# Performance work log

Measured on AMD Instinct MI355X. Metric: run time of the kernel, lower is better.

## Reference

```python
import jax, jax.numpy as jnp
import numpy as np

B, S, D, E, K = 4, 2048, 1024, 8, 2
H = 4 * D  # FFN hidden per expert


def setup_inputs() -> dict:
    key = jax.random.key(0)
    ks = jax.random.split(key, 5)
    s = 0.02  # init scale
    return {
        "x": jax.random.normal(ks[0], (B, S, D), dtype=jnp.float32),
        "Wg": jax.random.normal(ks[1], (D, E), dtype=jnp.float32) * s,
        "bg": jnp.zeros((E,), dtype=jnp.float32),
        "W1": jax.random.normal(ks[2], (E, D, H), dtype=jnp.float32) * s,
        "b1": jnp.zeros((E, H), dtype=jnp.float32),
        "W2": jax.random.normal(ks[3], (E, H, D), dtype=jnp.float32) * s,
        "b2": jnp.zeros((E, D), dtype=jnp.float32),
    }


def reference(x, Wg, bg, W1, b1, W2, b2):
    # Router: softmax over expert logits, then top-k (torch.topk semantics)
    probs = jax.nn.softmax(x @ Wg + bg, axis=-1)      # [B,S,E]
    w, idx = jax.lax.top_k(probs, K)                   # [B,S,K] each
    # Dense all-experts MLP (matches original: every expert runs on every token)
    h = jax.nn.gelu(jnp.einsum('bsd,edh->bseh', x, W1) + b1, approximate=False)  # [B,S,E,H]
    y = jnp.einsum('bseh,ehd->bsed', h, W2) + b2       # [B,S,E,D]
    # One-hot mask + weighted sum == gather selected experts, scale by w, sum over k
    yk = jnp.take_along_axis(y, idx[..., None], axis=2)  # [B,S,K,D]
    return jnp.sum(yk * w[..., None], axis=2)            # [B,S,D]
```

## Files before the change

### kernel.cpp

```cpp
#include <hip/hip_runtime.h>
#include <hip/hip_bf16.h>
#include <math.h>


#define TOK     8192
#define DMODEL  1024
#define NEXP    8
#define HFF     4096
#define NASSIGN 16384
#define SLOTPAD 16512
#define BM      128
#define BN      128
#define BK      32
#define MAXRT   135

typedef __attribute__((ext_vector_type(8))) short s16x8;
typedef __attribute__((ext_vector_type(4))) float f32x4;

__device__ __forceinline__ void gll16(const void* g, void* l) {
  __builtin_amdgcn_global_load_lds((const __attribute__((address_space(1))) void*)g,
                                   (__attribute__((address_space(3))) void*)l, 16, 0, 0);
}

__global__ void transpose_cvt(const float* __restrict__ in, __hip_bfloat16* __restrict__ out,
                              int R, int C) {
  __shared__ float t[64][65];
  const float* src = in + (size_t)blockIdx.z * R * C;
  __hip_bfloat16* dst = out + (size_t)blockIdx.z * R * C;
  const int r0 = blockIdx.y * 64, c0 = blockIdx.x * 64;
  const int tc = threadIdx.x & 63, tr = threadIdx.x >> 6;
#pragma unroll
  for (int i = 0; i < 16; ++i) {
    int r = i * 4 + tr;
    t[r][tc] = src[(size_t)(r0 + r) * C + c0 + tc];
  }
  __syncthreads();
#pragma unroll
  for (int i = 0; i < 16; ++i) {
    int rr = i * 4 + tr;
    dst[(size_t)(c0 + rr) * R + r0 + tc] = __float2bfloat16(t[tc][rr]);
  }
}

__global__ void router_kernel(const float* __restrict__ x, const float* __restrict__ Wg,
                              const float* __restrict__ bg, int* __restrict__ idx,
                              float* __restrict__ wtok, int* __restrict__ counts) {
  __shared__ int scnt[NEXP];
  if (threadIdx.x < NEXP) scnt[threadIdx.x] = 0;
  __syncthreads();
  const int wave = threadIdx.x >> 6, lane = threadIdx.x & 63;
  const int t = blockIdx.x * 4 + wave;
  float acc[NEXP];
#pragma unroll
  for (int e = 0; e < NEXP; ++e) acc[e] = 0.f;
  const float* xr = x + (size_t)t * DMODEL + lane * 16;
#pragma unroll
  for (int j = 0; j < 4; ++j) {
    float4 xv = *(const float4*)(xr + j * 4);
    const float* wr = Wg + (size_t)(lane * 16 + j * 4) * NEXP;
#pragma unroll
    for (int u = 0; u < 4; ++u) {
      float xs = (&xv.x)[u];
      float4 w0 = *(const float4*)(wr + u * NEXP);
      float4 w1 = *(const float4*)(wr + u * NEXP + 4);
      acc[0] += xs * w0.x; acc[1] += xs * w0.y; acc[2] += xs * w0.z; acc[3] += xs * w0.w;
      acc[4] += xs * w1.x; acc[5] += xs * w1.y; acc[6] += xs * w1.z; acc[7] += xs * w1.w;
    }
  }
#pragma unroll
  for (int off = 32; off >= 1; off >>= 1) {
#pragma unroll
    for (int e = 0; e < NEXP; ++e) acc[e] += __shfl_xor(acc[e], off, 64);
  }
  if (lane == 0) {
    float l[NEXP], m = -1e30f;
#pragma unroll
    for (int e = 0; e < NEXP; ++e) { l[e] = acc[e] + bg[e]; m = fmaxf(m, l[e]); }
    float p[NEXP], s = 0.f;
#pragma unroll
    for (int e = 0; e < NEXP; ++e) { p[e] = expf(l[e] - m); s += p[e]; }
    float inv = 1.f / s;
#pragma unroll
    for (int e = 0; e < NEXP; ++e) p[e] *= inv;
    int i0 = 0; float v0 = p[0];
#pragma unroll
    for (int e = 1; e < NEXP; ++e) if (p[e] > v0) { v0 = p[e]; i0 = e; }
    int i1 = -1; float v1 = -1e30f;
#pragma unroll
    for (int e = 0; e < NEXP; ++e) if (e != i0 && p[e] > v1) { v1 = p[e]; i1 = e; }
    idx[2 * t] = i0; idx[2 * t + 1] = i1;
    wtok[2 * t] = v0; wtok[2 * t + 1] = v1;
    atomicAdd(&scnt[i0], 1); atomicAdd(&scnt[i1], 1);
  }
  __syncthreads();
  if (threadIdx.x < NEXP) atomicAdd(&counts[threadIdx.x], scnt[threadIdx.x]);
}

__global__ void scan_kernel(int* ctrl) {
  if (threadIdx.x == 0 && blockIdx.x == 0) {
    int* counts = ctrl;
    int* cursor = ctrl + 8;
    int* expOff = ctrl + 16;
    int* tro = ctrl + 26;
    expOff[0] = 0; tro[0] = 0;
    for (int e = 0; e < NEXP; ++e) {
      expOff[e + 1] = expOff[e] + counts[e];
      tro[e + 1] = tro[e] + (counts[e] + BM - 1) / BM;
      cursor[e] = expOff[e];
    }
    ctrl[36] = tro[NEXP] * (HFF / BN);
    ctrl[37] = tro[NEXP] * (DMODEL / BN);
  }
}

__global__ void scatter_kernel(const int* __restrict__ idx, const float* __restrict__ wtok,
                               int* ctrl, int* __restrict__ perm, float* __restrict__ wslot,
                               int* __restrict__ inv) {
  __shared__ int lcnt[NEXP];
  __shared__ int lbase[NEXP];
  const int t = blockIdx.x * 256 + threadIdx.x;
  if (threadIdx.x < NEXP) lcnt[threadIdx.x] = 0;
  __syncthreads();
  const int e0 = idx[2 * t], e1 = idx[2 * t + 1];
  const int l0 = atomicAdd(&lcnt[e0], 1);
  const int l1 = atomicAdd(&lcnt[e1], 1);
  __syncthreads();
  if (threadIdx.x < NEXP)
    lbase[threadIdx.x] = atomicAdd(&ctrl[8 + threadIdx.x], lcnt[threadIdx.x]);
  __syncthreads();
  const int s0 = lbase[e0] + l0, s1 = lbase[e1] + l1;
  perm[s0] = t; perm[s1] = t;
  wslot[s0] = wtok[2 * t]; wslot[s1] = wtok[2 * t + 1];
  inv[2 * t] = s0; inv[2 * t + 1] = s1;
}

__global__ void gather_cvt_x(const float* __restrict__ x, const int* __restrict__ perm,
                             __hip_bfloat16* __restrict__ xg) {
  const int slot = blockIdx.x;
  const int t = perm[slot];
  const float4 v = *(const float4*)(x + (size_t)t * DMODEL + threadIdx.x * 4);
  union { ushort4 u; __hip_bfloat16 h[4]; } o;
  o.h[0] = __float2bfloat16(v.x); o.h[1] = __float2bfloat16(v.y);
  o.h[2] = __float2bfloat16(v.z); o.h[3] = __float2bfloat16(v.w);
  *(ushort4*)(xg + (size_t)slot * DMODEL + threadIdx.x * 4) = o.u;
}

__global__ __launch_bounds__(256, 2) void gemm1_kernel(
    const __hip_bfloat16* __restrict__ xg, const __hip_bfloat16* __restrict__ w1t,
    const float* __restrict__ b1, __hip_bfloat16* __restrict__ hbuf,
    const int* __restrict__ ctrl) {
  const int w = blockIdx.x;
  if (w >= ctrl[36]) return;
  const int* expOff = ctrl + 16;
  const int* tro = ctrl + 26;
  const int rt = w >> 5, nt = w & 31;
  int e = 0;
#pragma unroll
  for (int q = 1; q < NEXP; ++q) if (tro[q] <= rt) e = q;
  const int rowBase = expOff[e] + (rt - tro[e]) * BM;
  const int rowEnd = expOff[e + 1];

  __shared__ __hip_bfloat16 lA[BM * BK];
  __shared__ __hip_bfloat16 lB[BN * BK];

  const int tid = threadIdx.x;
  const int lane = tid & 63, wave = tid >> 6;
  const int quad = lane >> 4, lm = lane & 15;
  const int waveM = (wave >> 1) * 64, waveN = (wave & 1) * 64;

  f32x4 acc[4][4];
#pragma unroll
  for (int a = 0; a < 4; ++a)
#pragma unroll
    for (int b = 0; b < 4; ++b) acc[a][b] = (f32x4){0.f, 0.f, 0.f, 0.f};

  const int c0 = tid, c1 = tid + 256;
  const __hip_bfloat16* gA0 = xg + (size_t)(rowBase + (c0 >> 2)) * DMODEL + (c0 & 3) * 8;
  const __hip_bfloat16* gA1 = xg + (size_t)(rowBase + (c1 >> 2)) * DMODEL + (c1 & 3) * 8;
  const __hip_bfloat16* bbase = w1t + (size_t)e * HFF * DMODEL + (size_t)nt * BN * DMODEL;
  const __hip_bfloat16* gB0 = bbase + (size_t)(c0 >> 2) * DMODEL + (c0 & 3) * 8;
  const __hip_bfloat16* gB1 = bbase + (size_t)(c1 >> 2) * DMODEL + (c1 & 3) * 8;
  __hip_bfloat16* sA0 = lA + c0 * 8; __hip_bfloat16* sA1 = lA + c1 * 8;
  __hip_bfloat16* sB0 = lB + c0 * 8; __hip_bfloat16* sB1 = lB + c1 * 8;

  for (int kt = 0; kt < DMODEL / BK; ++kt) {
    gll16(gA0, sA0); gll16(gA1, sA1);
    gll16(gB0, sB0); gll16(gB1, sB1);
    gA0 += BK; gA1 += BK; gB0 += BK; gB1 += BK;
    __syncthreads();
    s16x8 af[4], bfr[4];
#pragma unroll
    for (int tm = 0; tm < 4; ++tm)
      af[tm] = *(const s16x8*)(lA + (waveM + tm * 16 + lm) * BK + quad * 8);
#pragma unroll
    for (int tn = 0; tn < 4; ++tn)
      bfr[tn] = *(const s16x8*)(lB + (waveN + tn * 16 + lm) * BK + quad * 8);
#pragma unroll
    for (int tm = 0; tm < 4; ++tm)
#pragma unroll
      for (int tn = 0; tn < 4; ++tn)
        acc[tm][tn] = __builtin_amdgcn_mfma_f32_16x16x32_bf16(af[tm], bfr[tn], acc[tm][tn], 0, 0, 0);
    __syncthreads();
  }

  const int colBase = nt * BN + waveN;
  float bv[4];
#pragma unroll
  for (int tn = 0; tn < 4; ++tn) bv[tn] = b1[e * HFF + colBase + tn * 16 + lm];
#pragma unroll
  for (int tm = 0; tm < 4; ++tm) {
    const int rb = rowBase + waveM + tm * 16 + quad * 4;
#pragma unroll
    for (int reg = 0; reg < 4; ++reg) {
      const int row = rb + reg;
      if (row < rowEnd) {
#pragma unroll
        for (int tn = 0; tn < 4; ++tn) {
          float v = acc[tm][tn][reg] + bv[tn];
          v = 0.5f * v * (1.f + erff(v * 0.70710678118654752f));
          hbuf[(size_t)row * HFF + colBase + tn * 16 + lm] = __float2bfloat16(v);
        }
      }
    }
  }
}

__global__ __launch_bounds__(256, 2) void gemm2_kernel(
    const __hip_bfloat16* __restrict__ hbuf, const __hip_bfloat16* __restrict__ w2t,
    const float* __restrict__ b2, const float* __restrict__ wslot,
    float* __restrict__ y, const int* __restrict__ ctrl) {
  const int w = blockIdx.x;
  if (w >= ctrl[37]) return;
  const int* expOff = ctrl + 16;
  const int* tro = ctrl + 26;
  const int rt = w >> 3, nt = w & 7;
  int e = 0;
#pragma unroll
  for (int q = 1; q < NEXP; ++q) if (tro[q] <= rt) e = q;
  const int rowBase = expOff[e] + (rt - tro[e]) * BM;
  const int rowEnd = expOff[e + 1];

  __shared__ __hip_bfloat16 lA[BM * BK];
  __shared__ __hip_bfloat16 lB[BN * BK];

  const int tid = threadIdx.x;
  const int lane = tid & 63, wave = tid >> 6;
  const int quad = lane >> 4, lm = lane & 15;
  const int waveM = (wave >> 1) * 64, waveN = (wave & 1) * 64;

  f32x4 acc[4][4];
#pragma unroll
  for (int a = 0; a < 4; ++a)
#pragma unroll
    for (int b = 0; b < 4; ++b) acc[a][b] = (f32x4){0.f, 0.f, 0.f, 0.f};

  const int c0 = tid, c1 = tid + 256;
  const __hip_bfloat16* gA0 = hbuf + (size_t)(rowBase + (c0 >> 2)) * HFF + (c0 & 3) * 8;
  const __hip_bfloat16* gA1 = hbuf + (size_t)(rowBase + (c1 >> 2)) * HFF + (c1 & 3) * 8;
  const __hip_bfloat16* bbase = w2t + (size_t)e * DMODEL * HFF + (size_t)nt * BN * HFF;
  const __hip_bfloat16* gB0 = bbase + (size_t)(c0 >> 2) * HFF + (c0 & 3) * 8;
  const __hip_bfloat16* gB1 = bbase + (size_t)(c1 >> 2) * HFF + (c1 & 3) * 8;
  __hip_bfloat16* sA0 = lA + c0 * 8; __hip_bfloat16* sA1 = lA + c1 * 8;
  __hip_bfloat16* sB0 = lB + c0 * 8; __hip_bfloat16* sB1 = lB + c1 * 8;

  for (int kt = 0; kt < HFF / BK; ++kt) {
    gll16(gA0, sA0); gll16(gA1, sA1);
    gll16(gB0, sB0); gll16(gB1, sB1);
    gA0 += BK; gA1 += BK; gB0 += BK; gB1 += BK;
    __syncthreads();
    s16x8 af[4], bfr[4];
#pragma unroll
    for (int tm = 0; tm < 4; ++tm)
      af[tm] = *(const s16x8*)(lA + (waveM + tm * 16 + lm) * BK + quad * 8);
#pragma unroll
    for (int tn = 0; tn < 4; ++tn)
      bfr[tn] = *(const s16x8*)(lB + (waveN + tn * 16 + lm) * BK + quad * 8);
#pragma unroll
    for (int tm = 0; tm < 4; ++tm)
#pragma unroll
      for (int tn = 0; tn < 4; ++tn)
        acc[tm][tn] = __builtin_amdgcn_mfma_f32_16x16x32_bf16(af[tm], bfr[tn], acc[tm][tn], 0, 0, 0);
    __syncthreads();
  }

  const int colBase = nt * BN + waveN;
  float bv[4];
#pragma unroll
  for (int tn = 0; tn < 4; ++tn) bv[tn] = b2[e * DMODEL + colBase + tn * 16 + lm];
#pragma unroll
  for (int tm = 0; tm < 4; ++tm) {
    const int rb = rowBase + waveM + tm * 16 + quad * 4;
#pragma unroll
    for (int reg = 0; reg < 4; ++reg) {
      const int row = rb + reg;
      if (row < rowEnd) {
        const float wr = wslot[row];
#pragma unroll
        for (int tn = 0; tn < 4; ++tn)
          y[(size_t)row * DMODEL + colBase + tn * 16 + lm] = (acc[tm][tn][reg] + bv[tn]) * wr;
      }
    }
  }
}

__global__ void combine_kernel(const float* __restrict__ y, const int* __restrict__ inv,
                               float* __restrict__ out) {
  const int t = blockIdx.x;
  const int s0 = inv[2 * t], s1 = inv[2 * t + 1];
  const int i = threadIdx.x * 4;
  float4 a = *(const float4*)(y + (size_t)s0 * DMODEL + i);
  float4 b = *(const float4*)(y + (size_t)s1 * DMODEL + i);
  float4 o;
  o.x = a.x + b.x; o.y = a.y + b.y; o.z = a.z + b.z; o.w = a.w + b.w;
  *(float4*)(out + (size_t)t * DMODEL + i) = o;
}

extern "C" void kernel_launch(void* const* d_in, const int* in_sizes, int n_in,
                              void* d_out, int out_size, void* d_ws, size_t ws_size,
                              hipStream_t stream) {
  const float* x  = (const float*)d_in[0];
  const float* Wg = (const float*)d_in[1];
  const float* bg = (const float*)d_in[2];
  const float* W1 = (const float*)d_in[3];
  const float* b1 = (const float*)d_in[4];
  const float* W2 = (const float*)d_in[5];
  const float* b2 = (const float*)d_in[6];
  float* out = (float*)d_out;

  char* ws = (char*)d_ws;
  size_t off = 0;
  auto take = [&](size_t bytes) -> char* {
    char* p = ws + off;
    off = (off + bytes + 255) & ~(size_t)255;
    return p;
  };
  int*   ctrl  = (int*)take(64 * sizeof(int));
  int*   idx   = (int*)take((size_t)TOK * 2 * 4);
  float* wtok  = (float*)take((size_t)TOK * 2 * 4);
  int*   perm  = (int*)take((size_t)SLOTPAD * 4);
  float* wslot = (float*)take((size_t)SLOTPAD * 4);
  int*   inv   = (int*)take((size_t)TOK * 2 * 4);
  __hip_bfloat16* W1t = (__hip_bfloat16*)take((size_t)NEXP * HFF * DMODEL * 2);
  __hip_bfloat16* W2t = (__hip_bfloat16*)take((size_t)NEXP * DMODEL * HFF * 2);
  __hip_bfloat16* xgb = (__hip_bfloat16*)take((size_t)SLOTPAD * DMODEL * 2);
  __hip_bfloat16* hb  = (__hip_bfloat16*)take((size_t)SLOTPAD * HFF * 2);
  float*          yb  = (float*)take((size_t)SLOTPAD * DMODEL * 4);
  (void)ws_size; (void)in_sizes; (void)n_in; (void)out_size;

  hipMemsetAsync(ctrl, 0, 64 * sizeof(int), stream);
  transpose_cvt<<<dim3(HFF / 64, DMODEL / 64, NEXP), 256, 0, stream>>>(W1, W1t, DMODEL, HFF);
  transpose_cvt<<<dim3(DMODEL / 64, HFF / 64, NEXP), 256, 0, stream>>>(W2, W2t, HFF, DMODEL);
  router_kernel<<<TOK / 4, 256, 0, stream>>>(x, Wg, bg, idx, wtok, ctrl);
  scan_kernel<<<1, 64, 0, stream>>>(ctrl);
  scatter_kernel<<<TOK / 256, 256, 0, stream>>>(idx, wtok, ctrl, perm, wslot, inv);
  gather_cvt_x<<<NASSIGN, 256, 0, stream>>>(x, perm, xgb);
  gemm1_kernel<<<MAXRT * (HFF / BN), 256, 0, stream>>>(xgb, W1t, b1, hb, ctrl);
  gemm2_kernel<<<MAXRT * (DMODEL / BN), 256, 0, stream>>>(hb, W2t, b2, wslot, yb, ctrl);
  combine_kernel<<<TOK, 256, 0, stream>>>(yb, inv, out);
}
```

Before: 853.7 us.

## Swizzle LDS tiles, reorder grid row-tile-major, raise occupancy, vectorize transpose stores

The GEMM kernels now apply an XOR-style rotation to the k-chunk position when loading A and B tiles into LDS, and read fragments through matching precomputed offsets, to cut LDS bank conflicts on the fragment reads. The grid is indexed with the row tile varying fastest (rt = w % MAXRT), so concurrently running blocks share weight column tiles, and the early-exit check now reads tro[NEXP] instead of the removed ctrl[36]/ctrl[37]. Launch bounds go from 2 to 4 blocks per SM, which may constrain registers. The transpose kernel now writes four bf16 values per store instead of one.

```diff
diff --git a/kernel.cpp b/kernel.cpp
--- a/kernel.cpp
+++ b/kernel.cpp
@@ -35,10 +35,15 @@
     t[r][tc] = src[(size_t)(r0 + r) * C + c0 + tc];
   }
   __syncthreads();
-#pragma unroll
-  for (int i = 0; i < 16; ++i) {
-    int rr = i * 4 + tr;
-    dst[(size_t)(c0 + rr) * R + r0 + tc] = __float2bfloat16(t[tc][rr]);
+  const int jl = (threadIdx.x & 15) * 4;
+  const int cw = threadIdx.x >> 4;
+#pragma unroll
+  for (int p = 0; p < 4; ++p) {
+    const int cc = p * 16 + cw;
+    union { ushort4 u; __hip_bfloat16 h[4]; } o;
+#pragma unroll
+    for (int u = 0; u < 4; ++u) o.h[u] = __float2bfloat16(t[jl + u][cc]);
+    *(ushort4*)(dst + (size_t)(c0 + cc) * R + r0 + jl) = o.u;
   }
 }
 
@@ -108,8 +113,6 @@
       tro[e + 1] = tro[e] + (counts[e] + BM - 1) / BM;
       cursor[e] = expOff[e];
     }
-    ctrl[36] = tro[NEXP] * (HFF / BN);
-    ctrl[37] = tro[NEXP] * (DMODEL / BN);
   }
 }
 
@@ -145,15 +148,16 @@
   *(ushort4*)(xg + (size_t)slot * DMODEL + threadIdx.x * 4) = o.u;
 }
 
-__global__ __launch_bounds__(256, 2) void gemm1_kernel(
+
+__global__ __launch_bounds__(256, 4) void gemm1_kernel(
     const __hip_bfloat16* __restrict__ xg, const __hip_bfloat16* __restrict__ w1t,
     const float* __restrict__ b1, __hip_bfloat16* __restrict__ hbuf,
     const int* __restrict__ ctrl) {
-  const int w = blockIdx.x;
-  if (w >= ctrl[36]) return;
   const int* expOff = ctrl + 16;
   const int* tro = ctrl + 26;
-  const int rt = w >> 5, nt = w & 31;
+  const int w = blockIdx.x;
+  const int rt = w % MAXRT, nt = w / MAXRT;
+  if (rt >= tro[NEXP]) return;
   int e = 0;
 #pragma unroll
   for (int q = 1; q < NEXP; ++q) if (tro[q] <= rt) e = q;
@@ -175,13 +179,28 @@
     for (int b = 0; b < 4; ++b) acc[a][b] = (f32x4){0.f, 0.f, 0.f, 0.f};
 
   const int c0 = tid, c1 = tid + 256;
-  const __hip_bfloat16* gA0 = xg + (size_t)(rowBase + (c0 >> 2)) * DMODEL + (c0 & 3) * 8;
-  const __hip_bfloat16* gA1 = xg + (size_t)(rowBase + (c1 >> 2)) * DMODEL + (c1 & 3) * 8;
+  const int rA0 = c0 >> 2, rA1 = c1 >> 2;
+  const int k0 = ((c0 & 3) - ((rA0 >> 1) & 3) + 4) & 3;
+  const int k1 = ((c1 & 3) - ((rA1 >> 1) & 3) + 4) & 3;
+  const __hip_bfloat16* gA0 = xg + (size_t)(rowBase + rA0) * DMODEL + k0 * 8;
+  const __hip_bfloat16* gA1 = xg + (size_t)(rowBase + rA1) * DMODEL + k1 * 8;
   const __hip_bfloat16* bbase = w1t + (size_t)e * HFF * DMODEL + (size_t)nt * BN * DMODEL;
-  const __hip_bfloat16* gB0 = bbase + (size_t)(c0 >> 2) * DMODEL + (c0 & 3) * 8;
-  const __hip_bfloat16* gB1 = bbase + (size_t)(c1 >> 2) * DMODEL + (c1 & 3) * 8;
+  const __hip_bfloat16* gB0 = bbase + (size_t)rA0 * DMODEL + k0 * 8;
+  const __hip_bfloat16* gB1 = bbase + (size_t)rA1 * DMODEL + k1 * 8;
   __hip_bfloat16* sA0 = lA + c0 * 8; __hip_bfloat16* sA1 = lA + c1 * 8;
   __hip_bfloat16* sB0 = lB + c0 * 8; __hip_bfloat16* sB1 = lB + c1 * 8;
+
+  int aOff[4], bOff[4];
+#pragma unroll
+  for (int tm = 0; tm < 4; ++tm) {
+    int r = waveM + tm * 16 + lm;
+    aOff[tm] = (r * 4 + ((quad + (r >> 1)) & 3)) * 8;
+  }
+#pragma unroll
+  for (int tn = 0; tn < 4; ++tn) {
+    int r = waveN + tn * 16 + lm;
+    bOff[tn] = (r * 4 + ((quad + (r >> 1)) & 3)) * 8;
+  }
 
   for (int kt = 0; kt < DMODEL / BK; ++kt) {
     gll16(gA0, sA0); gll16(gA1, sA1);
@@ -190,11 +209,9 @@
     __syncthreads();
     s16x8 af[4], bfr[4];
 #pragma unroll
-    for (int tm = 0; tm < 4; ++tm)
-      af[tm] = *(const s16x8*)(lA + (waveM + tm * 16 + lm) * BK + quad * 8);
-#pragma unroll
-    for (int tn = 0; tn < 4; ++tn)
-      bfr[tn] = *(const s16x8*)(lB + (waveN + tn * 16 + lm) * BK + quad * 8);
+    for (int tm = 0; tm < 4; ++tm) af[tm] = *(const s16x8*)(lA + aOff[tm]);
+#pragma unroll
+    for (int tn = 0; tn < 4; ++tn) bfr[tn] = *(const s16x8*)(lB + bOff[tn]);
 #pragma unroll
     for (int tm = 0; tm < 4; ++tm)
 #pragma unroll
@@ -225,15 +242,15 @@
   }
 }
 
-__global__ __launch_bounds__(256, 2) void gemm2_kernel(
+__global__ __launch_bounds__(256, 4) void gemm2_kernel(
     const __hip_bfloat16* __restrict__ hbuf, const __hip_bfloat16* __restrict__ w2t,
     const float* __restrict__ b2, const float* __restrict__ wslot,
     float* __restrict__ y, const int* __restrict__ ctrl) {
-  const int w = blockIdx.x;
-  if (w >= ctrl[37]) return;
   const int* expOff = ctrl + 16;
   const int* tro = ctrl + 26;
-  const int rt = w >> 3, nt = w & 7;
+  const int w = blockIdx.x;
+  const int rt = w % MAXRT, nt = w / MAXRT;
+  if (rt >= tro[NEXP]) return;
   int e = 0;
 #pragma unroll
   for (int q = 1; q < NEXP; ++q) if (tro[q] <= rt) e = q;
@@ -255,13 +272,28 @@
     for (int b = 0; b < 4; ++b) acc[a][b] = (f32x4){0.f, 0.f, 0.f, 0.f};
 
   const int c0 = tid, c1 = tid + 256;
-  const __hip_bfloat16* gA0 = hbuf + (size_t)(rowBase + (c0 >> 2)) * HFF + (c0 & 3) * 8;
-  const __hip_bfloat16* gA1 = hbuf + (size_t)(rowBase + (c1 >> 2)) * HFF + (c1 & 3) * 8;
+  const int rA0 = c0 >> 2, rA1 = c1 >> 2;
+  const int k0 = ((c0 & 3) - ((rA0 >> 1) & 3) + 4) & 3;
+  const int k1 = ((c1 & 3) - ((rA1 >> 1) & 3) + 4) & 3;
+  const __hip_bfloat16* gA0 = hbuf + (size_t)(rowBase + rA0) * HFF + k0 * 8;
+  const __hip_bfloat16* gA1 = hbuf + (size_t)(rowBase + rA1) * HFF + k1 * 8;
   const __hip_bfloat16* bbase = w2t + (size_t)e * DMODEL * HFF + (size_t)nt * BN * HFF;
-  const __hip_bfloat16* gB0 = bbase + (size_t)(c0 >> 2) * HFF + (c0 & 3) * 8;
-  const __hip_bfloat16* gB1 = bbase + (size_t)(c1 >> 2) * HFF + (c1 & 3) * 8;
+  const __hip_bfloat16* gB0 = bbase + (size_t)rA0 * HFF + k0 * 8;
+  const __hip_bfloat16* gB1 = bbase + (size_t)rA1 * HFF + k1 * 8;
   __hip_bfloat16* sA0 = lA + c0 * 8; __hip_bfloat16* sA1 = lA + c1 * 8;
   __hip_bfloat16* sB0 = lB + c0 * 8; __hip_bfloat16* sB1 = lB + c1 * 8;
+
+  int aOff[4], bOff[4];
+#pragma unroll
+  for (int tm = 0; tm < 4; ++tm) {
+    int r = waveM + tm * 16 + lm;
+    aOff[tm] = (r * 4 + ((quad + (r >> 1)) & 3)) * 8;
+  }
+#pragma unroll
+  for (int tn = 0; tn < 4; ++tn) {
+    int r = waveN + tn * 16 + lm;
+    bOff[tn] = (r * 4 + ((quad + (r >> 1)) & 3)) * 8;
+  }
 
   for (int kt = 0; kt < HFF / BK; ++kt) {
     gll16(gA0, sA0); gll16(gA1, sA1);
@@ -270,11 +302,9 @@
     __syncthreads();
     s16x8 af[4], bfr[4];
 #pragma unroll
-    for (int tm = 0; tm < 4; ++tm)
-      af[tm] = *(const s16x8*)(lA + (waveM + tm * 16 + lm) * BK + quad * 8);
-#pragma unroll
-    for (int tn = 0; tn < 4; ++tn)
-      bfr[tn] = *(const s16x8*)(lB + (waveN + tn * 16 + lm) * BK + quad * 8);
+    for (int tm = 0; tm < 4; ++tm) af[tm] = *(const s16x8*)(lA + aOff[tm]);
+#pragma unroll
+    for (int tn = 0; tn < 4; ++tn) bfr[tn] = *(const s16x8*)(lB + bOff[tn]);
 #pragma unroll
     for (int tm = 0; tm < 4; ++tm)
 #pragma unroll
```

Measured after the change: 1.058 ms. 24.0% more time.
